# Performance work log

Hardware: AMD Instinct MI355X
Metric: run time of the kernel (lower is better)

The kernel has to match this reference:

```python
import jax, jax.numpy as jnp
import numpy as np

BLOCKS, LAYERS, KS = 4, 2, 2
DILATIONS = [2 ** i for _ in range(BLOCKS) for i in range(LAYERS)]  # [1,2]*4
B, C_IN, N, T = 16, 2, 2048, 12
RC, DC, SC, EC, OUT = 32, 32, 256, 512, 12
L = BLOCKS * LAYERS
BN_EPS = 1e-5


def setup_inputs() -> dict:
    key = jax.random.key(0)
    ks = jax.random.split(key, 24)
    # raw inputs
    x = jax.random.normal(ks[0], (B, C_IN, N, T), dtype=jnp.float32)
    # two fixed supports: row-normalized random adjacency (dense, as in GraphWaveNet transition matrices)
    A_raw = jax.random.uniform(ks[1], (2, N, N), dtype=jnp.float32)
    A = A_raw / jnp.sum(A_raw, axis=2, keepdims=True)
    nodevec1 = jax.random.normal(ks[2], (N, 10), dtype=jnp.float32)
    nodevec2 = jax.random.normal(ks[3], (10, N), dtype=jnp.float32)
    s = 0.1  # weight scale to keep activations in a sane range
    filter_w = jax.random.normal(ks[4], (L, DC, RC, KS), dtype=jnp.float32) * s
    filter_b = jax.random.normal(ks[5], (L, DC), dtype=jnp.float32) * s
    gate_w = jax.random.normal(ks[6], (L, DC, RC, KS), dtype=jnp.float32) * s
    gate_b = jax.random.normal(ks[7], (L, DC), dtype=jnp.float32) * s
    skip_w = jax.random.normal(ks[8], (L, SC, DC), dtype=jnp.float32) * s
    skip_b = jax.random.normal(ks[9], (L, SC), dtype=jnp.float32) * s
    gcn_w = jax.random.normal(ks[10], (L, RC, 7 * DC), dtype=jnp.float32) * s
    gcn_b = jax.random.normal(ks[11], (L, RC), dtype=jnp.float32) * s
    bn_gamma = 1.0 + 0.1 * jax.random.normal(ks[12], (L, RC), dtype=jnp.float32)
    bn_beta = 0.1 * jax.random.normal(ks[13], (L, RC), dtype=jnp.float32)
    bn_mean = 0.1 * jax.random.normal(ks[14], (L, RC), dtype=jnp.float32)
    bn_var = 1.0 + jax.random.uniform(ks[15], (L, RC), dtype=jnp.float32)
    start_w = jax.random.normal(ks[16], (RC, C_IN), dtype=jnp.float32) * s
    start_b = jax.random.normal(ks[17], (RC,), dtype=jnp.float32) * s
    end1_w = jax.random.normal(ks[18], (EC, SC), dtype=jnp.float32) * s
    end1_b = jax.random.normal(ks[19], (EC,), dtype=jnp.float32) * s
    end2_w = jax.random.normal(ks[20], (OUT, EC), dtype=jnp.float32) * s
    end2_b = jax.random.normal(ks[21], (OUT,), dtype=jnp.float32) * s
    return dict(x=x, A=A, nodevec1=nodevec1, nodevec2=nodevec2,
                filter_w=filter_w, filter_b=filter_b, gate_w=gate_w, gate_b=gate_b,
                skip_w=skip_w, skip_b=skip_b, gcn_w=gcn_w, gcn_b=gcn_b,
                bn_gamma=bn_gamma, bn_beta=bn_beta, bn_mean=bn_mean, bn_var=bn_var,
                start_w=start_w, start_b=start_b, end1_w=end1_w, end1_b=end1_b,
                end2_w=end2_w, end2_b=end2_b)


def _conv1x1(x, w, b):
    # x: [b,c,n,t], w: [o,c] -> [b,o,n,t]
    return jnp.einsum('oc,bcnt->bont', w, x) + b[None, :, None, None]


def _dilated_conv2(x, w, b, d):
    # kernel (1,2) with time dilation d; out length T-d (valid conv)
    xa, xb = x[..., :-d], x[..., d:]
    y = jnp.einsum('oc,bcnt->bont', w[:, :, 0], xa) + jnp.einsum('oc,bcnt->bont', w[:, :, 1], xb)
    return y + b[None, :, None, None]


def _fwd(x, A, nodevec1, nodevec2, filter_w, filter_b, gate_w, gate_b,
         skip_w, skip_b, gcn_w, gcn_b, bn_gamma, bn_beta, bn_mean, bn_var,
         start_w, start_b, end1_w, end1_b, end2_w, end2_b):
    # pad 1 step at the start of time; T becomes 13 == receptive_field
    x = jnp.pad(x, ((0, 0), (0, 0), (0, 0), (1, 0)))
    x = x[:, :2]
    x = _conv1x1(x, start_w, start_b)  # [B,RC,N,13]
    # adaptive adjacency
    adp = jax.nn.softmax(jax.nn.relu(nodevec1 @ nodevec2), axis=1)
    supports = [A[0], A[1], adp]
    skip = None
    for i, d in enumerate(DILATIONS):
        residual = x
        filt = jnp.tanh(_dilated_conv2(residual, filter_w[i], filter_b[i], d))
        gate = jax.nn.sigmoid(_dilated_conv2(residual, gate_w[i], gate_b[i], d))
        x = filt * gate  # [B,DC,N,T-d]
        s = _conv1x1(x, skip_w[i], skip_b[i])  # [B,SC,N,T']
        skip = s if skip is None else s + skip[..., -s.shape[3]:]
        # GCN: order-2 diffusion over 3 supports, concat, 1x1 mix (dropout is identity in eval)
        outs = [x]
        for a in supports:
            x1 = jnp.einsum('bcvt,vw->bcwt', x, a)
            x2 = jnp.einsum('bcvt,vw->bcwt', x1, a)
            outs.extend([x1, x2])
        h = jnp.concatenate(outs, axis=1)  # [B,7*DC,N,T']
        x = _conv1x1(h, gcn_w[i], gcn_b[i])
        x = x + residual[..., -x.shape[3]:]
        # BatchNorm2d in eval mode (running stats)
        inv = bn_gamma[i] / jnp.sqrt(bn_var[i] + BN_EPS)
        x = (x - bn_mean[i][None, :, None, None]) * inv[None, :, None, None] + bn_beta[i][None, :, None, None]
    x = jax.nn.relu(skip)
    x = jax.nn.relu(_conv1x1(x, end1_w, end1_b))
    x = _conv1x1(x, end2_w, end2_b)  # [B,OUT,N,1]
    return x


def reference(x, A, nodevec1, nodevec2, filter_w, filter_b, gate_w, gate_b,
              skip_w, skip_b, gcn_w, gcn_b, bn_gamma, bn_beta, bn_mean, bn_var,
              start_w, start_b, end1_w, end1_b, end2_w, end2_b):
    return _fwd(x, A, nodevec1, nodevec2, filter_w, filter_b, gate_w, gate_b,
                skip_w, skip_b, gcn_w, gcn_b, bn_gamma, bn_beta, bn_mean, bn_var,
                start_w, start_b, end1_w, end1_b, end2_w, end2_b)
```

## Files before the change

### kernel.cpp

```cpp
#include <hip/hip_runtime.h>
#include <math.h>


#define NNODE 2048
#define NLAYER 8
#define SSTR ((size_t)NNODE * NNODE)

typedef unsigned short u16;
typedef unsigned int u32;
typedef __attribute__((ext_vector_type(8))) short bf16x8;
typedef __attribute__((ext_vector_type(4))) float f32x4;

__device__ __forceinline__ u16 f2bf(float f) {
    unsigned u = __builtin_bit_cast(unsigned, f);
    u += 0x7fffu + ((u >> 16) & 1u);
    return (u16)(u >> 16);
}
__device__ __forceinline__ float bf2f(u16 h) {
    unsigned u = ((unsigned)h) << 16;
    return __builtin_bit_cast(float, u);
}
__device__ __forceinline__ float bflo(u32 p) { return __builtin_bit_cast(float, p << 16); }
__device__ __forceinline__ float bfhi(u32 p) { return __builtin_bit_cast(float, p & 0xffff0000u); }
__device__ __forceinline__ u32 pack2(float a, float b) {
    return (u32)f2bf(a) | ((u32)f2bf(b) << 16);
}

__device__ __forceinline__ void gld16(const void* g, void* l) {
    __builtin_amdgcn_global_load_lds(
        (const __attribute__((address_space(1))) unsigned int*)g,
        (__attribute__((address_space(3))) unsigned int*)l, 16, 0, 0);
}

__global__ __launch_bounds__(256) void k_adp_mm(const float* __restrict__ nv1,
                                                const float* __restrict__ nv2,
                                                float* __restrict__ P) {
    int v = blockIdx.y;
    int w = blockIdx.x * 256 + threadIdx.x;
    float acc = 0.f;
#pragma unroll
    for (int k = 0; k < 10; ++k) acc += nv1[v * 10 + k] * nv2[k * NNODE + w];
    P[(size_t)v * NNODE + w] = acc;
}

__global__ __launch_bounds__(256) void k_softmax(float* __restrict__ P) {
    int v = blockIdx.x, tid = threadIdx.x;
    float* row = P + (size_t)v * NNODE;
    float m = 0.f;
    for (int w = tid; w < NNODE; w += 256) m = fmaxf(m, fmaxf(row[w], 0.f));
#pragma unroll
    for (int off = 32; off > 0; off >>= 1) m = fmaxf(m, __shfl_down(m, off));
    __shared__ float redm[4];
    __shared__ float reds[4];
    int wave = tid >> 6, lane = tid & 63;
    if (lane == 0) redm[wave] = m;
    __syncthreads();
    m = fmaxf(fmaxf(redm[0], redm[1]), fmaxf(redm[2], redm[3]));
    float s = 0.f;
    for (int w = tid; w < NNODE; w += 256) s += expf(fmaxf(row[w], 0.f) - m);
#pragma unroll
    for (int off = 32; off > 0; off >>= 1) s += __shfl_down(s, off);
    if (lane == 0) reds[wave] = s;
    __syncthreads();
    s = reds[0] + reds[1] + reds[2] + reds[3];
    float inv = 1.f / s;
    for (int w = tid; w < NNODE; w += 256) row[w] = expf(fmaxf(row[w], 0.f) - m) * inv;
}

__global__ __launch_bounds__(256) void k_transp(const float* __restrict__ A,
                                                const float* __restrict__ adp,
                                                u16* __restrict__ ST,
                                                u16* __restrict__ Sbf) {
    __shared__ float tile[32][33];
    int s = blockIdx.z;
    const float* src = (s < 2) ? (A + (size_t)s * SSTR) : adp;
    int v0 = blockIdx.y * 32, w0 = blockIdx.x * 32;
    int tx = threadIdx.x & 31, ty = threadIdx.x >> 5;
    u16* dst2 = Sbf + (size_t)s * SSTR;
#pragma unroll
    for (int p = 0; p < 4; ++p) {
        float v = src[(size_t)(v0 + ty + p * 8) * NNODE + w0 + tx];
        tile[ty + p * 8][tx] = v;
        dst2[(size_t)(v0 + ty + p * 8) * NNODE + w0 + tx] = f2bf(v);
    }
    __syncthreads();
    u16* dst = ST + (size_t)(2 * s) * SSTR;
#pragma unroll
    for (int p = 0; p < 4; ++p)
        dst[(size_t)(w0 + ty + p * 8) * NNODE + v0 + tx] = f2bf(tile[tx][ty + p * 8]);
}

__global__ __launch_bounds__(256) void k_gemm_mfma(
    const u16* __restrict__ A, int lda, size_t asstr,
    const u16* __restrict__ BT, size_t bsstr,
    u16* __restrict__ C, int ldc, size_t csstr, int sbase) {
    __shared__ u16 Asl[128 * 32];
    __shared__ u16 Bsl[128 * 32];
    const int tid = threadIdx.x;
    const int wave = tid >> 6, lane = tid & 63;
    const int sidx = sbase + blockIdx.z;
    const u16* Ab = A + sidx * asstr + (size_t)blockIdx.y * 128 * lda;
    const u16* Bb = BT + sidx * bsstr + (size_t)blockIdx.x * 128 * NNODE;
    const int tr = tid >> 2;
    const int tc = (tid & 3) * 8;
    char* AslB = (char*)Asl + wave * 1024;
    char* BslB = (char*)Bsl + wave * 1024;
    const int wm = (wave & 1) * 64, wn = (wave >> 1) * 64;
    const int fr = lane & 15;
    const int fk = (lane >> 4) * 8;
    f32x4 acc[4][4];
#pragma unroll
    for (int i = 0; i < 4; ++i)
#pragma unroll
        for (int j = 0; j < 4; ++j) acc[i][j] = (f32x4){0.f, 0.f, 0.f, 0.f};

    for (int k0 = 0; k0 < 2048; k0 += 32) {
        gld16(Ab + (size_t)tr * lda + k0 + tc, AslB);
        gld16(Ab + (size_t)(tr + 64) * lda + k0 + tc, AslB + 4096);
        gld16(Bb + (size_t)tr * NNODE + k0 + tc, BslB);
        gld16(Bb + (size_t)(tr + 64) * NNODE + k0 + tc, BslB + 4096);
        __syncthreads();
        bf16x8 af[4], bf[4];
#pragma unroll
        for (int i = 0; i < 4; ++i)
            af[i] = *(const bf16x8*)&Asl[(wm + i * 16 + fr) * 32 + fk];
#pragma unroll
        for (int j = 0; j < 4; ++j)
            bf[j] = *(const bf16x8*)&Bsl[(wn + j * 16 + fr) * 32 + fk];
#pragma unroll
        for (int i = 0; i < 4; ++i)
#pragma unroll
            for (int j = 0; j < 4; ++j)
                acc[i][j] = __builtin_amdgcn_mfma_f32_16x16x32_bf16(af[i], bf[j], acc[i][j], 0, 0, 0);
        __syncthreads();
    }
    u16* Cb = C + sidx * csstr + (size_t)(blockIdx.y * 128 + wm) * ldc + blockIdx.x * 128 + wn;
    const int orow = (lane >> 4) * 4;
#pragma unroll
    for (int i = 0; i < 4; ++i)
#pragma unroll
        for (int j = 0; j < 4; ++j)
#pragma unroll
            for (int r = 0; r < 4; ++r)
                Cb[(size_t)(i * 16 + orow + r) * ldc + j * 16 + fr] = f2bf(acc[i][j][r]);
}

__global__ __launch_bounds__(512, 2) void k_gemmZ(const u16* __restrict__ Xg,
                                                  const u16* __restrict__ ST,
                                                  u16* __restrict__ Z, int pass) {
    __shared__ __align__(16) char ldsb[131072];
    const int tid = threadIdx.x;
    const int wave = tid >> 6, lane = tid & 63;
    const int m0 = blockIdx.y * 256;
    const int slice = pass * 3 + (blockIdx.x >> 3);
    const int n0 = (blockIdx.x & 7) * 256;
    const u16* AbG = Xg + (size_t)m0 * 2048;
    const u16* BbG = ST + (size_t)slice * SSTR + (size_t)n0 * 2048;

    const int xorc = ((tid & 7) ^ ((tid >> 3) & 7)) << 3;
    const size_t aRow = (size_t)(tid >> 3) * 2048 + xorc;
    const int bRowLoc = ((tid >> 8) << 6) + (((tid >> 6) & 3) << 3) + ((tid >> 3) & 7);
    const size_t bRow = (size_t)bRowLoc * 2048 + xorc;
    const int aw = wave << 10;
    const int bw = ((wave >> 2) << 13) + ((wave & 3) << 10);

    const int fr = lane & 15;
    const int cl4 = lane >> 4;
    const int ch0 = (cl4 ^ (fr & 7)) << 4;
    const int ch1 = ch0 ^ 64;
    const int aRd = ((wave & 1) << 14) + fr * 128;
    const int bRd = ((wave >> 1) << 13) + fr * 128;
    const int wm = (wave & 1) << 7;
    const int wn = (wave >> 1) << 6;

    char* A0 = ldsb;
    char* A1 = ldsb + 32768;
    char* B0 = ldsb + 65536;
    char* B1 = ldsb + 98304;

    auto STA = [&](char* Abase, int k0, int q) {
        const size_t g = (size_t)(q << 6) * 2048 + aRow + k0;
        gld16(AbG + g, Abase + (q << 13) + aw);
        gld16(AbG + g + (size_t)128 * 2048, Abase + 16384 + (q << 13) + aw);
    };
    auto STB = [&](char* Bbase, int k0, int q) {
        const size_t g = (size_t)(q << 5) * 2048 + bRow + k0;
        gld16(BbG + g, Bbase + (q << 12) + bw);
        gld16(BbG + g + (size_t)128 * 2048, Bbase + 16384 + (q << 12) + bw);
    };

    f32x4 acc[8][4];
#pragma unroll
    for (int i = 0; i < 8; ++i)
#pragma unroll
        for (int j = 0; j < 4; ++j) acc[i][j] = (f32x4){0.f, 0.f, 0.f, 0.f};

    STA(A0, 0, 0); STA(A0, 0, 1); STB(B0, 0, 0); STB(B0, 0, 1);
    STA(A1, 64, 0); STB(B1, 64, 0); STB(B1, 64, 1);
    asm volatile("s_waitcnt vmcnt(6)" ::: "memory");
    asm volatile("s_barrier" ::: "memory");

    char *Ac = A0, *Ao = A1, *Bc = B0, *Bo = B1;
    bf16x8 af[4][2], bfl[2][2], bfh[2][2];

    for (int T = 0; T < 32; ++T) {
#pragma unroll
        for (int i = 0; i < 4; ++i) {
            af[i][0] = *(const bf16x8*)(Ac + aRd + (i << 11) + ch0);
            af[i][1] = *(const bf16x8*)(Ac + aRd + (i << 11) + ch1);
        }
#pragma unroll
        for (int j = 0; j < 2; ++j) {
            bfl[j][0] = *(const bf16x8*)(Bc + bRd + (j << 11) + ch0);
            bfl[j][1] = *(const bf16x8*)(Bc + bRd + (j << 11) + ch1);
        }
        if (T < 31) STA(Ao, (T + 1) * 64, 1);
        asm volatile("s_barrier" ::: "memory");
        asm volatile("s_waitcnt lgkmcnt(0)" ::: "memory");
        __builtin_amdgcn_sched_barrier(0);
        __builtin_amdgcn_s_setprio(1);
#pragma unroll
        for (int i = 0; i < 4; ++i)
#pragma unroll
            for (int j = 0; j < 2; ++j) {
                acc[i][j] = __builtin_amdgcn_mfma_f32_16x16x32_bf16(af[i][0], bfl[j][0], acc[i][j], 0, 0, 0);
                acc[i][j] = __builtin_amdgcn_mfma_f32_16x16x32_bf16(af[i][1], bfl[j][1], acc[i][j], 0, 0, 0);
            }
        __builtin_amdgcn_s_setprio(0);
#pragma unroll
        for (int j = 0; j < 2; ++j) {
            bfh[j][0] = *(const bf16x8*)(Bc + bRd + 4096 + (j << 11) + ch0);
            bfh[j][1] = *(const bf16x8*)(Bc + bRd + 4096 + (j << 11) + ch1);
        }
        asm volatile("s_barrier" ::: "memory");
        asm volatile("s_waitcnt lgkmcnt(0)" ::: "memory");
        __builtin_amdgcn_sched_barrier(0);
        __builtin_amdgcn_s_setprio(1);
#pragma unroll
        for (int i = 0; i < 4; ++i)
#pragma unroll
            for (int j = 0; j < 2; ++j) {
                acc[i][2 + j] = __builtin_amdgcn_mfma_f32_16x16x32_bf16(af[i][0], bfh[j][0], acc[i][2 + j], 0, 0, 0);
                acc[i][2 + j] = __builtin_amdgcn_mfma_f32_16x16x32_bf16(af[i][1], bfh[j][1], acc[i][2 + j], 0, 0, 0);
            }
        __builtin_amdgcn_s_setprio(0);
#pragma unroll
        for (int i = 0; i < 4; ++i) {
            af[i][0] = *(const bf16x8*)(Ac + aRd + 8192 + (i << 11) + ch0);
            af[i][1] = *(const bf16x8*)(Ac + aRd + 8192 + (i << 11) + ch1);
        }
        if (T < 30) { STA(Ac, (T + 2) * 64, 0); STB(Bc, (T + 2) * 64, 0); }
        asm volatile("s_barrier" ::: "memory");
        asm volatile("s_waitcnt lgkmcnt(0)" ::: "memory");
        __builtin_amdgcn_sched_barrier(0);
        __builtin_amdgcn_s_setprio(1);
#pragma unroll
        for (int i = 0; i < 4; ++i)
#pragma unroll
            for (int j = 0; j < 2; ++j) {
                acc[4 + i][2 + j] = __builtin_amdgcn_mfma_f32_16x16x32_bf16(af[i][0], bfh[j][0], acc[4 + i][2 + j], 0, 0, 0);
                acc[4 + i][2 + j] = __builtin_amdgcn_mfma_f32_16x16x32_bf16(af[i][1], bfh[j][1], acc[4 + i][2 + j], 0, 0, 0);
            }
        __builtin_amdgcn_s_setprio(0);
        if (T < 30) STB(Bc, (T + 2) * 64, 1);
        asm volatile("s_barrier" ::: "memory");
        __builtin_amdgcn_sched_barrier(0);
        __builtin_amdgcn_s_setprio(1);
#pragma unroll
        for (int i = 0; i < 4; ++i)
#pragma unroll
            for (int j = 0; j < 2; ++j) {
                acc[4 + i][j] = __builtin_amdgcn_mfma_f32_16x16x32_bf16(af[i][0], bfl[j][0], acc[4 + i][j], 0, 0, 0);
                acc[4 + i][j] = __builtin_amdgcn_mfma_f32_16x16x32_bf16(af[i][1], bfl[j][1], acc[4 + i][j], 0, 0, 0);
            }
        __builtin_amdgcn_s_setprio(0);
        if (T < 30) {
            asm volatile("s_waitcnt vmcnt(6)" ::: "memory");
        } else if (T == 30) {
            asm volatile("s_waitcnt vmcnt(0)" ::: "memory");
        }
        asm volatile("s_barrier" ::: "memory");
        char* t;
        t = Ac; Ac = Ao; Ao = t;
        t = Bc; Bc = Bo; Bo = t;
    }

    const int col0 = (blockIdx.x >> 3) * 2048 + (blockIdx.x & 7) * 256;
    u16* Cb = Z + (size_t)(m0 + wm) * 6144 + col0 + wn;
    const int orow = cl4 * 4;
#pragma unroll
    for (int i = 0; i < 8; ++i)
#pragma unroll
        for (int j = 0; j < 4; ++j)
#pragma unroll
            for (int r = 0; r < 4; ++r)
                Cb[(size_t)(i * 16 + orow + r) * 6144 + j * 16 + fr] = f2bf(acc[i][j][r]);
}

__global__ __launch_bounds__(256) void k_gemmZ128(const u16* __restrict__ Xg,
                                                  const u16* __restrict__ ST,
                                                  u16* __restrict__ Z, int pass) {
    __shared__ u16 Asl[2][128 * 32];
    __shared__ u16 Bsl[2][128 * 32];
    const int tid = threadIdx.x;
    const int wave = tid >> 6, lane = tid & 63;
    const int m0 = blockIdx.y * 128;
    const int slice = pass * 3 + (blockIdx.x >> 4);
    const int nIn = (blockIdx.x & 15) * 128;
    const u16* Ab = Xg + (size_t)m0 * 2048;
    const u16* Bb = ST + (size_t)slice * SSTR + (size_t)nIn * NNODE;
    const int tr = tid >> 2;
    const int tc = (tid & 3) * 8;
    char* AslB0 = (char*)Asl[0] + wave * 1024;
    char* AslB1 = (char*)Asl[1] + wave * 1024;
    char* BslB0 = (char*)Bsl[0] + wave * 1024;
    char* BslB1 = (char*)Bsl[1] + wave * 1024;
    const int wm = (wave & 1) * 64, wn = (wave >> 1) * 64;
    const int fr = lane & 15;
    const int fk = (lane >> 4) * 8;
    f32x4 acc[4][4];
#pragma unroll
    for (int i = 0; i < 4; ++i)
#pragma unroll
        for (int j = 0; j < 4; ++j) acc[i][j] = (f32x4){0.f, 0.f, 0.f, 0.f};

    for (int k0 = 0; k0 < 2048; k0 += 64) {
        gld16(Ab + (size_t)tr * 2048 + k0 + tc, AslB0);
        gld16(Ab + (size_t)(tr + 64) * 2048 + k0 + tc, AslB0 + 4096);
        gld16(Ab + (size_t)tr * 2048 + k0 + 32 + tc, AslB1);
        gld16(Ab + (size_t)(tr + 64) * 2048 + k0 + 32 + tc, AslB1 + 4096);
        gld16(Bb + (size_t)tr * NNODE + k0 + tc, BslB0);
        gld16(Bb + (size_t)(tr + 64) * NNODE + k0 + tc, BslB0 + 4096);
        gld16(Bb + (size_t)tr * NNODE + k0 + 32 + tc, BslB1);
        gld16(Bb + (size_t)(tr + 64) * NNODE + k0 + 32 + tc, BslB1 + 4096);
        __syncthreads();
#pragma unroll
        for (int h = 0; h < 2; ++h) {
            bf16x8 af[4], bf[4];
#pragma unroll
            for (int i = 0; i < 4; ++i)
                af[i] = *(const bf16x8*)&Asl[h][(wm + i * 16 + fr) * 32 + fk];
#pragma unroll
            for (int j = 0; j < 4; ++j)
                bf[j] = *(const bf16x8*)&Bsl[h][(wn + j * 16 + fr) * 32 + fk];
#pragma unroll
            for (int i = 0; i < 4; ++i)
#pragma unroll
                for (int j = 0; j < 4; ++j)
                    acc[i][j] = __builtin_amdgcn_mfma_f32_16x16x32_bf16(af[i], bf[j], acc[i][j], 0, 0, 0);
        }
        __syncthreads();
    }
    u16* Cb = Z + (size_t)(m0 + wm) * 6144 + blockIdx.x * 128 + wn;
    const int orow = (lane >> 4) * 4;
#pragma unroll
    for (int i = 0; i < 4; ++i)
#pragma unroll
        for (int j = 0; j < 4; ++j)
#pragma unroll
            for (int r = 0; r < 4; ++r)
                Cb[(size_t)(i * 16 + orow + r) * 6144 + j * 16 + fr] = f2bf(acc[i][j][r]);
}

__global__ __launch_bounds__(256) void k_start(const float* __restrict__ xin,
                                               const float* __restrict__ sw,
                                               const float* __restrict__ sb,
                                               u16* __restrict__ out, int b0) {
    int n = blockIdx.x * 256 + threadIdx.x;
    int t = blockIdx.y;
    int bl = blockIdx.z;
    int b = b0 + bl;
    float x0 = 0.f, x1 = 0.f;
    if (t > 0) {
        x0 = xin[((size_t)(b * 2 + 0) * NNODE + n) * 12 + (t - 1)];
        x1 = xin[((size_t)(b * 2 + 1) * NNODE + n) * 12 + (t - 1)];
    }
#pragma unroll
    for (int co = 0; co < 32; ++co) {
        float v = sw[co * 2 + 0] * x0 + sw[co * 2 + 1] * x1 + sb[co];
        out[((size_t)(bl * 32 + co) * 13 + t) * NNODE + n] = f2bf(v);
    }
}

__global__ __launch_bounds__(256) void k_gate(const u16* __restrict__ cur,
                                              u16* __restrict__ xg,
                                              u16* __restrict__ nxt,
                                              int T, int Tn, int d,
                                              const float* __restrict__ fw,
                                              const float* __restrict__ fb,
                                              const float* __restrict__ gw,
                                              const float* __restrict__ gb,
                                              const float* __restrict__ gcwl,
                                              const float* __restrict__ gcbl,
                                              int donxt) {
    __shared__ float4 wp[1024];
    __shared__ float w0[32][33];
    int tid = threadIdx.x;
#pragma unroll
    for (int u = 0; u < 4; ++u) {
        int idx = tid + u * 256;
        int ci = idx >> 5, co = idx & 31;
        wp[idx] = make_float4(fw[co * 64 + ci * 2], fw[co * 64 + ci * 2 + 1],
                              gw[co * 64 + ci * 2], gw[co * 64 + ci * 2 + 1]);
        w0[ci][co] = gcwl[co * 224 + ci];
    }
    __syncthreads();
    int n = blockIdx.x * 512 + tid * 2;
    int t = blockIdx.y;
    int bl = blockIdx.z;
    float f0[32], f1[32], g0[32], g1[32];
#pragma unroll
    for (int co = 0; co < 32; ++co) { f0[co] = 0.f; f1[co] = 0.f; g0[co] = 0.f; g1[co] = 0.f; }
    for (int ci = 0; ci < 32; ++ci) {
        size_t ba = ((size_t)(bl * 32 + ci) * T + t) * NNODE + n;
        size_t bb = ((size_t)(bl * 32 + ci) * T + t + d) * NNODE + n;
        u32 ua = *(const u32*)&cur[ba];
        u32 ub = *(const u32*)&cur[bb];
        float xa0 = bflo(ua), xa1 = bfhi(ua);
        float xb0 = bflo(ub), xb1 = bfhi(ub);
#pragma unroll
        for (int co = 0; co < 32; ++co) {
            float4 w = wp[ci * 32 + co];
            f0[co] += w.x * xa0 + w.y * xb0;
            f1[co] += w.x * xa1 + w.y * xb1;
            g0[co] += w.z * xa0 + w.w * xb0;
            g1[co] += w.z * xa1 + w.w * xb1;
        }
    }
#pragma unroll
    for (int co = 0; co < 32; ++co) {
        float fbv = fb[co], gbv = gb[co];
        float a0 = tanhf(f0[co] + fbv) * (1.f / (1.f + expf(-(g0[co] + gbv))));
        float a1 = tanhf(f1[co] + fbv) * (1.f / (1.f + expf(-(g1[co] + gbv))));
        f0[co] = a0; f1[co] = a1;
        size_t o = ((size_t)(bl * 32 + co) * Tn + t) * NNODE + n;
        *(u32*)&xg[o] = pack2(a0, a1);
    }
    if (donxt) {
#pragma unroll
        for (int cop = 0; cop < 32; ++cop) {
            float s0 = gcbl[cop], s1 = s0;
#pragma unroll
            for (int ci = 0; ci < 32; ++ci) {
                float wv = w0[ci][cop];
                s0 += wv * f0[ci];
                s1 += wv * f1[ci];
            }
            size_t o = ((size_t)(bl * 32 + cop) * Tn + t) * NNODE + n;
            *(u32*)&nxt[o] = pack2(s0, s1);
        }
    }
}

__global__ __launch_bounds__(256) void k_skip(const u16* __restrict__ xg,
                                              float* __restrict__ skip, int Tn,
                                              const float* __restrict__ sw,
                                              const float* __restrict__ sb, int b0, int init) {
    __shared__ float wl[256];
    int tid = threadIdx.x;
    int sc0 = blockIdx.y * 8;
    wl[tid] = sw[sc0 * 32 + tid];
    __syncthreads();
    int n = blockIdx.x * 512 + tid * 2;
    int bl = blockIdx.z;
    float a0[8], a1[8];
#pragma unroll
    for (int j = 0; j < 8; ++j) { a0[j] = 0.f; a1[j] = 0.f; }
    for (int ci = 0; ci < 32; ci += 2) {
        u32 p0 = *(const u32*)&xg[((size_t)(bl * 32 + ci + 0) * Tn + (Tn - 1)) * NNODE + n];
        u32 p1 = *(const u32*)&xg[((size_t)(bl * 32 + ci + 1) * Tn + (Tn - 1)) * NNODE + n];
        float v00 = bflo(p0), v01 = bfhi(p0);
        float v10 = bflo(p1), v11 = bfhi(p1);
#pragma unroll
        for (int j = 0; j < 8; ++j) {
            float wA = wl[j * 32 + ci], wB = wl[j * 32 + ci + 1];
            a0[j] += wA * v00 + wB * v10;
            a1[j] += wA * v01 + wB * v11;
        }
    }
    int b = b0 + bl;
#pragma unroll
    for (int j = 0; j < 8; ++j) {
        size_t o = ((size_t)(b * 256) + sc0 + j) * NNODE + n;
        float bsv = sb[sc0 + j];
        if (init) {
            *(float2*)&skip[o] = make_float2(a0[j] + bsv, a1[j] + bsv);
        } else {
            float2 old = *(const float2*)&skip[o];
            *(float2*)&skip[o] = make_float2(old.x + a0[j] + bsv, old.y + a1[j] + bsv);
        }
    }
}

__global__ __launch_bounds__(256) void k_accum(const u16* __restrict__ Z,
                                               int cbase,
                                               const float* __restrict__ gcnw,
                                               u16* __restrict__ outp,
                                               const u16* __restrict__ resid,
                                               int Tn, int d, int finalf,
                                               const float* __restrict__ bng,
                                               const float* __restrict__ bnb,
                                               const float* __restrict__ bnm,
                                               const float* __restrict__ bnv) {
    __shared__ float wl[3][32][32];
    int tid = threadIdx.x;
    for (int u = tid; u < 3072; u += 256) {
        int g = u >> 10, ci = (u >> 5) & 31, co = u & 31;
        wl[g][ci][co] = gcnw[co * 224 + cbase + g * 32 + ci];
    }
    __syncthreads();
    int n = blockIdx.x * 512 + tid * 2;
    int t = blockIdx.y, bl = blockIdx.z;
    float a0[32], a1[32];
#pragma unroll
    for (int co = 0; co < 32; ++co) { a0[co] = 0.f; a1[co] = 0.f; }
    for (int ci = 0; ci < 32; ++ci) {
        size_t m = (size_t)(bl * 32 + ci) * Tn + t;
#pragma unroll
        for (int g = 0; g < 3; ++g) {
            u32 zz = *(const u32*)&Z[m * 6144 + g * 2048 + n];
            float v0 = bflo(zz), v1 = bfhi(zz);
#pragma unroll
            for (int cq = 0; cq < 8; ++cq) {
                float4 w = *(const float4*)&wl[g][ci][cq * 4];
                a0[cq * 4 + 0] += w.x * v0; a1[cq * 4 + 0] += w.x * v1;
                a0[cq * 4 + 1] += w.y * v0; a1[cq * 4 + 1] += w.y * v1;
                a0[cq * 4 + 2] += w.z * v0; a1[cq * 4 + 2] += w.z * v1;
                a0[cq * 4 + 3] += w.w * v0; a1[cq * 4 + 3] += w.w * v1;
            }
        }
    }
#pragma unroll
    for (int co = 0; co < 32; ++co) {
        size_t o = ((size_t)(bl * 32 + co) * Tn + t) * NNODE + n;
        u32 oo = *(const u32*)&outp[o];
        float v0 = bflo(oo) + a0[co];
        float v1 = bfhi(oo) + a1[co];
        if (finalf) {
            size_t ro = ((size_t)(bl * 32 + co) * (Tn + d) + t + d) * NNODE + n;
            u32 rr = *(const u32*)&resid[ro];
            v0 += bflo(rr); v1 += bfhi(rr);
            float inv = bng[co] * rsqrtf(bnv[co] + 1e-5f);
            float mu = bnm[co], be = bnb[co];
            v0 = (v0 - mu) * inv + be;
            v1 = (v1 - mu) * inv + be;
        }
        *(u32*)&outp[o] = pack2(v0, v1);
    }
}

__global__ __launch_bounds__(256) void k_skipT(const float* __restrict__ skip,
                                               u16* __restrict__ skipT) {
    __shared__ float tile[32][33];
    int b = blockIdx.z;
    int n0 = blockIdx.x * 32, c0 = blockIdx.y * 32;
    int tx = threadIdx.x & 31, ty = threadIdx.x >> 5;
#pragma unroll
    for (int p = 0; p < 4; ++p)
        tile[ty + p * 8][tx] = skip[((size_t)b * 256 + c0 + ty + p * 8) * NNODE + n0 + tx];
    __syncthreads();
#pragma unroll
    for (int p = 0; p < 4; ++p)
        skipT[((size_t)b * NNODE + n0 + ty + p * 8) * 256 + c0 + tx] =
            f2bf(fmaxf(tile[tx][ty + p * 8], 0.f));
}

__global__ __launch_bounds__(256) void k_cast(const float* __restrict__ src,
                                              u16* __restrict__ dst) {
    int i = blockIdx.x * 256 + threadIdx.x;
    dst[i] = f2bf(src[i]);
}

__global__ __launch_bounds__(256) void k_end1m(const u16* __restrict__ E1,
                                               const u16* __restrict__ skT,
                                               const float* __restrict__ bias,
                                               u16* __restrict__ h) {
    __shared__ u16 Asl[128 * 32];
    __shared__ u16 Bsl[128 * 32];
    const int tid = threadIdx.x;
    const int wave = tid >> 6, lane = tid & 63;
    const int b = blockIdx.z;
    const int m0 = blockIdx.y * 128;
    const int n0 = blockIdx.x * 128;
    const int tr = tid >> 2;
    const int tc = (tid & 3) * 8;
    char* AslB = (char*)Asl + wave * 1024;
    char* BslB = (char*)Bsl + wave * 1024;
    const int wm = (wave & 1) * 64, wn = (wave >> 1) * 64;
    const int fr = lane & 15;
    const int fk = (lane >> 4) * 8;
    const u16* Ab = E1 + (size_t)m0 * 256;
    const u16* Bb = skT + ((size_t)b * NNODE + n0) * 256;
    f32x4 acc[4][4];
#pragma unroll
    for (int i = 0; i < 4; ++i)
#pragma unroll
        for (int j = 0; j < 4; ++j) acc[i][j] = (f32x4){0.f, 0.f, 0.f, 0.f};
    for (int k0 = 0; k0 < 256; k0 += 32) {
        gld16(Ab + (size_t)tr * 256 + k0 + tc, AslB);
        gld16(Ab + (size_t)(tr + 64) * 256 + k0 + tc, AslB + 4096);
        gld16(Bb + (size_t)tr * 256 + k0 + tc, BslB);
        gld16(Bb + (size_t)(tr + 64) * 256 + k0 + tc, BslB + 4096);
        __syncthreads();
        bf16x8 af[4], bf[4];
#pragma unroll
        for (int i = 0; i < 4; ++i)
            af[i] = *(const bf16x8*)&Asl[(wm + i * 16 + fr) * 32 + fk];
#pragma unroll
        for (int j = 0; j < 4; ++j)
            bf[j] = *(const bf16x8*)&Bsl[(wn + j * 16 + fr) * 32 + fk];
#pragma unroll
        for (int i = 0; i < 4; ++i)
#pragma unroll
            for (int j = 0; j < 4; ++j)
                acc[i][j] = __builtin_amdgcn_mfma_f32_16x16x32_bf16(af[i], bf[j], acc[i][j], 0, 0, 0);
        __syncthreads();
    }
    const int orow = (lane >> 4) * 4;
#pragma unroll
    for (int i = 0; i < 4; ++i)
#pragma unroll
        for (int r = 0; r < 4; ++r) {
            int m = m0 + wm + i * 16 + orow + r;
            float bs = bias[m];
            size_t ob = ((size_t)b * 512 + m) * NNODE + n0 + wn;
#pragma unroll
            for (int j = 0; j < 4; ++j)
                h[ob + j * 16 + fr] = f2bf(fmaxf(acc[i][j][r] + bs, 0.f));
        }
}

__global__ __launch_bounds__(256) void k_end2(const u16* __restrict__ h,
                                              const float* __restrict__ w,
                                              const float* __restrict__ bias,
                                              float* __restrict__ out) {
    __shared__ float wl[12][512];
    int tid = threadIdx.x;
    for (int u = tid; u < 6144; u += 256) wl[u >> 9][u & 511] = w[u];
    __syncthreads();
    int n = blockIdx.x * 256 + tid;
    int b = blockIdx.y;
    float acc[12];
#pragma unroll
    for (int o = 0; o < 12; ++o) acc[o] = 0.f;
#pragma unroll 4
    for (int e = 0; e < 512; ++e) {
        float v = bf2f(h[((size_t)(b * 512) + e) * NNODE + n]);
#pragma unroll
        for (int o = 0; o < 12; ++o) acc[o] += wl[o][e] * v;
    }
#pragma unroll
    for (int o = 0; o < 12; ++o)
        out[((size_t)(b * 12) + o) * NNODE + n] = acc[o] + bias[o];
}

extern "C" void kernel_launch(void* const* d_in, const int* in_sizes, int n_in,
                              void* d_out, int out_size, void* d_ws, size_t ws_size,
                              hipStream_t stream) {
    const float* x_in = (const float*)d_in[0];
    const float* A    = (const float*)d_in[1];
    const float* nv1  = (const float*)d_in[2];
    const float* nv2  = (const float*)d_in[3];
    const float* fw   = (const float*)d_in[4];
    const float* fb   = (const float*)d_in[5];
    const float* gw   = (const float*)d_in[6];
    const float* gb   = (const float*)d_in[7];
    const float* skw  = (const float*)d_in[8];
    const float* skb  = (const float*)d_in[9];
    const float* gcw  = (const float*)d_in[10];
    const float* gcb  = (const float*)d_in[11];
    const float* bng  = (const float*)d_in[12];
    const float* bnb  = (const float*)d_in[13];
    const float* bnm  = (const float*)d_in[14];
    const float* bnv  = (const float*)d_in[15];
    const float* stw  = (const float*)d_in[16];
    const float* stb  = (const float*)d_in[17];
    const float* e1w  = (const float*)d_in[18];
    const float* e1b  = (const float*)d_in[19];
    const float* e2w  = (const float*)d_in[20];
    const float* e2b  = (const float*)d_in[21];
    (void)in_sizes; (void)n_in; (void)out_size;

    const int BL = (ws_size >= 239075328UL) ? 16 : 8;
    const int nch = 16 / BL;
    const size_t bufsz = (size_t)BL * 1703936UL;

    char* base = (char*)d_ws;
    u16*   ST   = (u16*)base;
    float* skip = (float*)(base + 50331648UL);
    u16*   bufA = (u16*)(base + 83886080UL);
    u16*   bufB = (u16*)(base + 83886080UL + bufsz);
    u16*   xg   = (u16*)(base + 83886080UL + 2 * bufsz);
    u16*   Z    = (u16*)(base + 83886080UL + 2 * bufsz + (size_t)BL * 1572864UL);
    float* adp  = (float*)Z;
    u16*   Sbf  = (u16*)bufA;
    u16*   h     = (u16*)(base + 83886080UL);
    u16*   skipT = (u16*)(base + 83886080UL + 33554432UL);
    u16*   E1bf  = (u16*)ST;

    k_adp_mm<<<dim3(8, 2048), 256, 0, stream>>>(nv1, nv2, adp);
    k_softmax<<<2048, 256, 0, stream>>>(adp);
    k_transp<<<dim3(64, 64, 3), 256, 0, stream>>>(A, adp, ST, Sbf);
    k_gemm_mfma<<<dim3(16, 16, 3), 256, 0, stream>>>(
        ST, NNODE, 2 * SSTR, Sbf, SSTR, ST + SSTR, NNODE, 2 * SSTR, 0);

    static const int DIL[NLAYER] = {1, 2, 1, 2, 1, 2, 1, 2};
    for (int ch = 0; ch < nch; ++ch) {
        int b0 = ch * BL;
        k_start<<<dim3(8, 13, BL), 256, 0, stream>>>(x_in, stw, stb, bufA, b0);
        u16* cur = bufA;
        u16* nxt = bufB;
        int T = 13;
        for (int i = 0; i < NLAYER; ++i) {
            int d = DIL[i], Tn = T - d;
            int last = (i == NLAYER - 1);
            k_gate<<<dim3(4, Tn, BL), 256, 0, stream>>>(cur, xg, nxt, T, Tn, d,
                fw + i * 2048, fb + i * 32, gw + i * 2048, gb + i * 32,
                gcw + i * 32 * 224, gcb + i * 32, last ? 0 : 1);
            k_skip<<<dim3(4, 32, BL), 256, 0, stream>>>(xg, skip, Tn,
                skw + i * 256 * 32, skb + i * 256, b0, (i == 0) ? 1 : 0);
            if (last) break;
            const float* gcwi = gcw + i * 32 * 224;
            for (int p = 0; p < 2; ++p) {
                if (Tn == 6 || Tn == 3) {
                    k_gemmZ128<<<dim3(48, BL * Tn / 4), 256, 0, stream>>>(xg, ST, Z, p);
                } else {
                    k_gemmZ<<<dim3(24, BL * 32 * Tn / 256), 512, 0, stream>>>(xg, ST, Z, p);
                }
                k_accum<<<dim3(4, Tn, BL), 256, 0, stream>>>(
                    Z, 32 + 96 * p, gcwi, nxt, cur, Tn, d, p,
                    bng + i * 32, bnb + i * 32, bnm + i * 32, bnv + i * 32);
            }
            u16* tmp = cur; cur = nxt; nxt = tmp;
            T = Tn;
        }
    }
    k_cast<<<512, 256, 0, stream>>>(e1w, E1bf);
    k_skipT<<<dim3(64, 8, 16), 256, 0, stream>>>(skip, skipT);
    k_end1m<<<dim3(16, 4, 16), 256, 0, stream>>>(E1bf, skipT, e1b, h);
    k_end2<<<dim3(8, 16), 256, 0, stream>>>(h, e2w, e2b, (float*)d_out);
}
```

Measured before the change: 3.023 ms.

## Replace per-layer skip convolutions with one batched MFMA GEMM over stacked layer outputs

The gate kernel now writes each layer's last-timestep activations in bf16 into a node-major buffer with 8 layers times 32 channels. A single MFMA GEMM at the end computes all skip convolutions at once, adds the pre-summed biases and applies ReLU, writing the transposed bf16 skip tensor directly. This removes the eight fp32 read-modify-write passes over the skip accumulator and the separate transpose kernel. In exchange there are strided scalar stores in the gate kernel, and the skip contributions are summed in bf16 inputs rather than fp32.

```diff
diff --git a/kernel.cpp b/kernel.cpp
--- a/kernel.cpp
+++ b/kernel.cpp
@@ -88,6 +88,21 @@
 #pragma unroll
     for (int p = 0; p < 4; ++p)
         dst[(size_t)(w0 + ty + p * 8) * NNODE + v0 + tx] = f2bf(tile[tx][ty + p * 8]);
+}
+
+__global__ __launch_bounds__(256) void k_skprep(const float* __restrict__ skw,
+                                                const float* __restrict__ skb,
+                                                u16* __restrict__ skwB,
+                                                float* __restrict__ skbsum) {
+    int idx = blockIdx.x * 256 + threadIdx.x;
+    int sc = idx >> 8, k = idx & 255, l = k >> 5, ci = k & 31;
+    skwB[idx] = f2bf(skw[((size_t)l * 256 + sc) * 32 + ci]);
+    if (blockIdx.x == 0) {
+        float s = 0.f;
+#pragma unroll
+        for (int ll = 0; ll < 8; ++ll) s += skb[ll * 256 + threadIdx.x];
+        skbsum[threadIdx.x] = s;
+    }
 }
 
 __global__ __launch_bounds__(256) void k_gemm_mfma(
@@ -392,7 +407,8 @@
                                               const float* __restrict__ gb,
                                               const float* __restrict__ gcwl,
                                               const float* __restrict__ gcbl,
-                                              int donxt) {
+                                              u16* __restrict__ xl,
+                                              int layer, int donxt) {
     __shared__ float4 wp[1024];
     __shared__ float w0[32][33];
     int tid = threadIdx.x;
@@ -436,6 +452,14 @@
         size_t o = ((size_t)(bl * 32 + co) * Tn + t) * NNODE + n;
         *(u32*)&xg[o] = pack2(a0, a1);
     }
+    if (t == Tn - 1) {
+        size_t o2 = ((size_t)(bl * 2048 + n)) * 256 + layer * 32;
+#pragma unroll
+        for (int co = 0; co < 32; ++co) {
+            xl[o2 + co] = f2bf(f0[co]);
+            xl[o2 + 256 + co] = f2bf(f1[co]);
+        }
+    }
     if (donxt) {
 #pragma unroll
         for (int cop = 0; cop < 32; ++cop) {
@@ -448,46 +472,6 @@
             }
             size_t o = ((size_t)(bl * 32 + cop) * Tn + t) * NNODE + n;
             *(u32*)&nxt[o] = pack2(s0, s1);
-        }
-    }
-}
-
-__global__ __launch_bounds__(256) void k_skip(const u16* __restrict__ xg,
-                                              float* __restrict__ skip, int Tn,
-                                              const float* __restrict__ sw,
-                                              const float* __restrict__ sb, int b0, int init) {
-    __shared__ float wl[256];
-    int tid = threadIdx.x;
-    int sc0 = blockIdx.y * 8;
-    wl[tid] = sw[sc0 * 32 + tid];
-    __syncthreads();
-    int n = blockIdx.x * 512 + tid * 2;
-    int bl = blockIdx.z;
-    float a0[8], a1[8];
-#pragma unroll
-    for (int j = 0; j < 8; ++j) { a0[j] = 0.f; a1[j] = 0.f; }
-    for (int ci = 0; ci < 32; ci += 2) {
-        u32 p0 = *(const u32*)&xg[((size_t)(bl * 32 + ci + 0) * Tn + (Tn - 1)) * NNODE + n];
-        u32 p1 = *(const u32*)&xg[((size_t)(bl * 32 + ci + 1) * Tn + (Tn - 1)) * NNODE + n];
-        float v00 = bflo(p0), v01 = bfhi(p0);
-        float v10 = bflo(p1), v11 = bfhi(p1);
-#pragma unroll
-        for (int j = 0; j < 8; ++j) {
-            float wA = wl[j * 32 + ci], wB = wl[j * 32 + ci + 1];
-            a0[j] += wA * v00 + wB * v10;
-            a1[j] += wA * v01 + wB * v11;
-        }
-    }
-    int b = b0 + bl;
-#pragma unroll
-    for (int j = 0; j < 8; ++j) {
-        size_t o = ((size_t)(b * 256) + sc0 + j) * NNODE + n;
-        float bsv = sb[sc0 + j];
-        if (init) {
-            *(float2*)&skip[o] = make_float2(a0[j] + bsv, a1[j] + bsv);
-        } else {
-            float2 old = *(const float2*)&skip[o];
-            *(float2*)&skip[o] = make_float2(old.x + a0[j] + bsv, old.y + a1[j] + bsv);
         }
     }
 }
@@ -549,26 +533,69 @@
     }
 }
 
-__global__ __launch_bounds__(256) void k_skipT(const float* __restrict__ skip,
-                                               u16* __restrict__ skipT) {
-    __shared__ float tile[32][33];
-    int b = blockIdx.z;
-    int n0 = blockIdx.x * 32, c0 = blockIdx.y * 32;
-    int tx = threadIdx.x & 31, ty = threadIdx.x >> 5;
-#pragma unroll
-    for (int p = 0; p < 4; ++p)
-        tile[ty + p * 8][tx] = skip[((size_t)b * 256 + c0 + ty + p * 8) * NNODE + n0 + tx];
-    __syncthreads();
-#pragma unroll
-    for (int p = 0; p < 4; ++p)
-        skipT[((size_t)b * NNODE + n0 + ty + p * 8) * 256 + c0 + tx] =
-            f2bf(fmaxf(tile[tx][ty + p * 8], 0.f));
-}
-
 __global__ __launch_bounds__(256) void k_cast(const float* __restrict__ src,
                                               u16* __restrict__ dst) {
     int i = blockIdx.x * 256 + threadIdx.x;
     dst[i] = f2bf(src[i]);
+}
+
+__global__ __launch_bounds__(256) void k_skipg(const u16* __restrict__ xl,
+                                               const u16* __restrict__ skwB,
+                                               const float* __restrict__ skbsum,
+                                               u16* __restrict__ skipT) {
+    __shared__ u16 Asl[128 * 32];
+    __shared__ u16 Bsl[128 * 32];
+    const int tid = threadIdx.x;
+    const int wave = tid >> 6, lane = tid & 63;
+    const int m0 = blockIdx.y * 128;
+    const int n0 = blockIdx.x * 128;
+    const int tr = tid >> 2;
+    const int tc = (tid & 3) * 8;
+    char* AslB = (char*)Asl + wave * 1024;
+    char* BslB = (char*)Bsl + wave * 1024;
+    const int wm = (wave & 1) * 64, wn = (wave >> 1) * 64;
+    const int fr = lane & 15;
+    const int fk = (lane >> 4) * 8;
+    const u16* Ab = xl + (size_t)m0 * 256;
+    const u16* Bb = skwB + (size_t)n0 * 256;
+    f32x4 acc[4][4];
+#pragma unroll
+    for (int i = 0; i < 4; ++i)
+#pragma unroll
+        for (int j = 0; j < 4; ++j) acc[i][j] = (f32x4){0.f, 0.f, 0.f, 0.f};
+    for (int k0 = 0; k0 < 256; k0 += 32) {
+        gld16(Ab + (size_t)tr * 256 + k0 + tc, AslB);
+        gld16(Ab + (size_t)(tr + 64) * 256 + k0 + tc, AslB + 4096);
+        gld16(Bb + (size_t)tr * 256 + k0 + tc, BslB);
+        gld16(Bb + (size_t)(tr + 64) * 256 + k0 + tc, BslB + 4096);
+        __syncthreads();
+        bf16x8 af[4], bf[4];
+#pragma unroll
+        for (int i = 0; i < 4; ++i)
+            af[i] = *(const bf16x8*)&Asl[(wm + i * 16 + fr) * 32 + fk];
+#pragma unroll
+        for (int j = 0; j < 4; ++j)
+            bf[j] = *(const bf16x8*)&Bsl[(wn + j * 16 + fr) * 32 + fk];
+#pragma unroll
+        for (int i = 0; i < 4; ++i)
+#pragma unroll
+            for (int j = 0; j < 4; ++j)
+                acc[i][j] = __builtin_amdgcn_mfma_f32_16x16x32_bf16(af[i], bf[j], acc[i][j], 0, 0, 0);
+        __syncthreads();
+    }
+    const int orow = (lane >> 4) * 4;
+#pragma unroll
+    for (int i = 0; i < 4; ++i)
+#pragma unroll
+        for (int r = 0; r < 4; ++r) {
+            int m = m0 + wm + i * 16 + orow + r;
+            size_t ob = (size_t)m * 256 + n0 + wn;
+#pragma unroll
+            for (int j = 0; j < 4; ++j) {
+                int col = n0 + wn + j * 16 + fr;
+                skipT[ob + j * 16 + fr] = f2bf(fmaxf(acc[i][j][r] + skbsum[col], 0.f));
+            }
+        }
 }
 
 __global__ __launch_bounds__(256) void k_end1m(const u16* __restrict__ E1,
@@ -686,8 +713,10 @@
     const size_t bufsz = (size_t)BL * 1703936UL;
 
     char* base = (char*)d_ws;
-    u16*   ST   = (u16*)base;
-    float* skip = (float*)(base + 50331648UL);
+    u16*   ST     = (u16*)base;
+    u16*   xlast  = (u16*)(base + 50331648UL);
+    u16*   skwB   = (u16*)(base + 67108864UL);
+    float* skbsum = (float*)(base + 67239936UL);
     u16*   bufA = (u16*)(base + 83886080UL);
     u16*   bufB = (u16*)(base + 83886080UL + bufsz);
     u16*   xg   = (u16*)(base + 83886080UL + 2 * bufsz);
@@ -699,6 +728,7 @@
     u16*   E1bf  = (u16*)ST;
 
     k_adp_mm<<<dim3(8, 2048), 256, 0, stream>>>(nv1, nv2, adp);
+    k_skprep<<<256, 256, 0, stream>>>(skw, skb, skwB, skbsum);
     k_softmax<<<2048, 256, 0, stream>>>(adp);
     k_transp<<<dim3(64, 64, 3), 256, 0, stream>>>(A, adp, ST, Sbf);
     k_gemm_mfma<<<dim3(16, 16, 3), 256, 0, stream>>>(
@@ -716,27 +746,31 @@
             int last = (i == NLAYER - 1);
             k_gate<<<dim3(4, Tn, BL), 256, 0, stream>>>(cur, xg, nxt, T, Tn, d,
                 fw + i * 2048, fb + i * 32, gw + i * 2048, gb + i * 32,
-                gcw + i * 32 * 224, gcb + i * 32, last ? 0 : 1);
-            k_skip<<<dim3(4, 32, BL), 256, 0, stream>>>(xg, skip, Tn,
-                skw + i * 256 * 32, skb + i * 256, b0, (i == 0) ? 1 : 0);
+                gcw + i * 32 * 224, gcb + i * 32,
+                xlast + (size_t)b0 * 2048 * 256, i, last ? 0 : 1);
             if (last) break;
             const float* gcwi = gcw + i * 32 * 224;
-            for (int p = 0; p < 2; ++p) {
-                if (Tn == 6 || Tn == 3) {
+            if (Tn == 6 || Tn == 3) {
+                for (int p = 0; p < 2; ++p) {
                     k_gemmZ128<<<dim3(48, BL * Tn / 4), 256, 0, stream>>>(xg, ST, Z, p);
-                } else {
+                    k_accum<<<dim3(4, Tn, BL), 256, 0, stream>>>(
+                        Z, 32 + 96 * p, gcwi, nxt, cur, Tn, d, p,
+                        bng + i * 32, bnb + i * 32, bnm + i * 32, bnv + i * 32);
+                }
+            } else {
+                for (int p = 0; p < 2; ++p) {
                     k_gemmZ<<<dim3(24, BL * 32 * Tn / 256), 512, 0, stream>>>(xg, ST, Z, p);
+                    k_accum<<<dim3(4, Tn, BL), 256, 0, stream>>>(
+                        Z, 32 + 96 * p, gcwi, nxt, cur, Tn, d, p,
+                        bng + i * 32, bnb + i * 32, bnm + i * 32, bnv + i * 32);
                 }
-                k_accum<<<dim3(4, Tn, BL), 256, 0, stream>>>(
-                    Z, 32 + 96 * p, gcwi, nxt, cur, Tn, d, p,
-                    bng + i * 32, bnb + i * 32, bnm + i * 32, bnv + i * 32);
             }
             u16* tmp = cur; cur = nxt; nxt = tmp;
             T = Tn;
         }
     }
     k_cast<<<512, 256, 0, stream>>>(e1w, E1bf);
-    k_skipT<<<dim3(64, 8, 16), 256, 0, stream>>>(skip, skipT);
+    k_skipg<<<dim3(2, 256), 256, 0, stream>>>(xlast, skwB, skbsum, skipT);
     k_end1m<<<dim3(16, 4, 16), 256, 0, stream>>>(E1bf, skipT, e1b, h);
     k_end2<<<dim3(8, 16), 256, 0, stream>>>(h, e2w, e2b, (float*)d_out);
 }
```

New measurement: 2.985 ms. Within noise of the previous version (-1.2%).
